# Kernel tuning notes

Hardware: AMD Instinct MI355X
Metric: run time of the kernel (lower is better)

The kernel has to match this reference:

```python
import jax, jax.numpy as jnp
import numpy as np
from jax import lax

KERNEL_SIZE = 15

def _gabor_kernels(theta, sigma, lambd, gamma, psi):
    # Vectorized kernel generation over orientations. Grid is a fixed buffer.
    half = KERNEL_SIZE // 2
    r = jnp.arange(-half, half + 1, dtype=jnp.float32)
    yg, xg = jnp.meshgrid(r, r, indexing='ij')          # [k, k]
    th = theta[:, None, None]                            # [O,1,1]
    sg = jnp.clip(sigma, 1.0, None)[:, None, None]
    lb = jnp.clip(lambd, 2.0, None)[:, None, None]
    gm = jnp.clip(gamma, 0.1, 1.0)[:, None, None]
    ps = psi[:, None, None]
    ct, st = jnp.cos(th), jnp.sin(th)
    x_th = xg * ct + yg * st                             # [O,k,k]
    y_th = -xg * st + yg * ct
    gaussian = jnp.exp(-0.5 * (x_th**2 + gm**2 * y_th**2) / sg**2)
    sinusoid = jnp.cos(2.0 * np.pi * x_th / lb + ps)
    k = gaussian * sinusoid
    k = k - k.mean(axis=(1, 2), keepdims=True)
    # torch.std is unbiased (ddof=1)
    k = k / (k.std(axis=(1, 2), keepdims=True, ddof=1) + 1e-8)
    return k[:, None, :, :]                              # [O,1,k,k]

def setup_inputs() -> dict:
    key = jax.random.key(0)
    O, ks = 8, KERNEL_SIZE
    x = jax.random.normal(key, (64, 3, 256, 256), dtype=jnp.float32)
    theta = jnp.linspace(0.0, np.pi, O + 1)[:-1].astype(jnp.float32)
    sigma = jnp.ones((O,), jnp.float32) * (ks / 4.0)
    lambd = jnp.ones((O,), jnp.float32) * (ks / 2.0)
    gamma = jnp.ones((O,), jnp.float32) * 0.5
    psi = jnp.zeros((O,), jnp.float32)
    return {"x": x, "theta": theta, "sigma": sigma, "lambd": lambd,
            "gamma": gamma, "psi": psi}

def reference(x, theta, sigma, lambd, gamma, psi):
    # sum_i conv2d(x[:,i:i+1], K) == conv2d(sum_i x[:,i:i+1], K) since the
    # same kernels are applied to every channel and conv is linear.
    kernels = _gabor_kernels(theta, sigma, lambd, gamma, psi)  # [O,1,k,k]
    xs = x.sum(axis=1, keepdims=True)                          # [B,1,H,W]
    pad = KERNEL_SIZE // 2
    out = lax.conv_general_dilated(
        xs, kernels,
        window_strides=(1, 1),
        padding=[(pad, pad), (pad, pad)],
        dimension_numbers=('NCHW', 'OIHW', 'NCHW'))
    return out  # [B, O, H, W]
```

## Files before the change

kernel.cpp:

```cpp
#include <hip/hip_runtime.h>
#include <math.h>

#define KS    15
#define HALF  7
#define NORI  8
#define HW    256
#define TW    64
#define TH    64
#define WT    96
#define WROW  48
#define RT    80
#define TWORDS (RT * WROW)

typedef __attribute__((ext_vector_type(8))) short  short8;
typedef __attribute__((ext_vector_type(4))) float  floatx4;

union FragU { uint4 u4; short8 s8; };

__device__ __forceinline__ ushort f2bf(float f) {
    union { float f; uint u; } a; a.f = f;
    return (ushort)((a.u + 0x7FFFu + ((a.u >> 16) & 1u)) >> 16);
}

__global__ __launch_bounds__(256) void gabor_mfma(
    const float* __restrict__ x,
    const float* __restrict__ theta, const float* __restrict__ sigma,
    const float* __restrict__ lambd, const float* __restrict__ gamma,
    const float* __restrict__ psi,
    float* __restrict__ out)
{
    __shared__ uint   tile[2 * TWORDS];
    __shared__ ushort kwa[16 * 16 * 16];

    const int tid  = threadIdx.x;
    const int img  = blockIdx.z;
    const int h0   = blockIdx.y * TH;
    const int w0   = blockIdx.x * TW;
    const int lane = tid & 63;
    const int wave = tid >> 6;

    for (int i = tid; i < 16 * 16 * 16; i += 256) kwa[i] = 0;
    __syncthreads();

    #pragma unroll 1
    for (int oo = 0; oo < 2; ++oo) {
        const int o = wave * 2 + oo;
        const float th = theta[o];
        const float sg = fmaxf(sigma[o], 1.0f);
        const float lb = fmaxf(lambd[o], 2.0f);
        const float gm = fminf(fmaxf(gamma[o], 0.1f), 1.0f);
        const float ps = psi[o];
        const float ct = cosf(th), st = sinf(th);
        const float inv_sg2 = 1.0f / (sg * sg);
        const float gm2 = gm * gm;
        const float wfreq = 6.283185307179586f / lb;

        float vals[4];
        float sum = 0.0f, sumsq = 0.0f;
        #pragma unroll
        for (int j = 0; j < 4; ++j) {
            const int t = lane + j * 64;
            float v = 0.0f;
            if (t < KS * KS) {
                const int ky = t / KS, kx = t % KS;
                const float yg = (float)(ky - HALF);
                const float xg = (float)(kx - HALF);
                const float x_th =  xg * ct + yg * st;
                const float y_th = -xg * st + yg * ct;
                const float g = expf(-0.5f * (x_th * x_th + gm2 * y_th * y_th) * inv_sg2);
                v = g * cosf(wfreq * x_th + ps);
                sum += v; sumsq += v * v;
            }
            vals[j] = v;
        }
        #pragma unroll
        for (int off = 32; off > 0; off >>= 1) {
            sum   += __shfl_down(sum,   off);
            sumsq += __shfl_down(sumsq, off);
        }
        sum = __shfl(sum, 0); sumsq = __shfl(sumsq, 0);
        const float nn   = (float)(KS * KS);
        const float mean = sum / nn;
        const float var  = (sumsq - sum * sum / nn) / (nn - 1.0f);
        const float inv  = 1.0f / (sqrtf(var) + 1e-8f);
        #pragma unroll
        for (int j = 0; j < 4; ++j) {
            const int t = lane + j * 64;
            if (t < KS * KS) {
                const int ky = t / KS, kx = t % KS;
                kwa[(o * 16 + ky) * 16 + kx] = f2bf((vals[j] - mean) * inv);
            }
        }
    }

    {
        const float* xim = x + ((size_t)img * 3) * HW * HW;
        for (int i = tid; i < 2 * TWORDS; i += 256) {
            const int s  = (i >= TWORDS) ? 1 : 0;
            const int j  = i - s * TWORDS;
            const int r  = j / WROW, wc = j - r * WROW;
            const int h  = h0 + r - HALF;
            const int wb = w0 + 2 * wc + s - HALF;
            float v0 = 0.0f, v1 = 0.0f;
            if (h >= 0 && h < HW) {
                const float* xr = xim + h * HW;
                if (wb >= 0 && wb < HW)
                    v0 = xr[wb] + xr[wb + HW * HW] + xr[wb + 2 * HW * HW];
                const int wb1 = wb + 1;
                if (wb1 >= 0 && wb1 < HW)
                    v1 = xr[wb1] + xr[wb1 + HW * HW] + xr[wb1 + 2 * HW * HW];
            }
            tile[i] = (uint)f2bf(v0) | ((uint)f2bf(v1) << 16);
        }
    }
    __syncthreads();

    const int q  = lane >> 4;
    const int n  = lane & 15;
    const int qh = q >> 1;
    const int kx0 = 8 * (q & 1);

    short8 afrag[8];
    #pragma unroll
    for (int c = 0; c < 8; ++c) {
        const int ky = 2 * c + qh;
        afrag[c] = *reinterpret_cast<const short8*>(&kwa[((n * 16 + ky) * 16) + kx0]);
    }

    const int pc   = wave * 16;
    const int col0 = pc + n + kx0;
    const int s    = col0 & 1;
    const int cw   = col0 >> 1;
    const uint cbase = (uint)(s * TWORDS + cw);

    #pragma unroll 1
    for (int it = 0; it < 8; ++it) {
        const int pr0 = it * 8;
        floatx4 acc_e[4], acc_o[4];
        #pragma unroll
        for (int i = 0; i < 4; ++i) { acc_e[i] = (floatx4){0,0,0,0}; acc_o[i] = (floatx4){0,0,0,0}; }

        const uint base0 = cbase + (uint)((pr0 + qh) * WROW);
        #pragma unroll
        for (int t = 0; t < 11; ++t) {
            const uint oe = base0 + (uint)(2 * t * WROW);
            FragU fe, fo;
            fe.u4.x = tile[oe + 0]; fe.u4.y = tile[oe + 1];
            fe.u4.z = tile[oe + 2]; fe.u4.w = tile[oe + 3];
            fo.u4.x = tile[oe + WROW + 0]; fo.u4.y = tile[oe + WROW + 1];
            fo.u4.z = tile[oe + WROW + 2]; fo.u4.w = tile[oe + WROW + 3];
            #pragma unroll
            for (int i = 0; i < 4; ++i) {
                if (t - i >= 0 && t - i < 8) {
                    acc_e[i] = __builtin_amdgcn_mfma_f32_16x16x32_bf16(afrag[t - i], fe.s8, acc_e[i], 0, 0, 0);
                    acc_o[i] = __builtin_amdgcn_mfma_f32_16x16x32_bf16(afrag[t - i], fo.s8, acc_o[i], 0, 0, 0);
                }
            }
        }

        if (q < 2) {
            const int wcol = w0 + pc + n;
            float* ob = out + (((size_t)img * NORI + q * 4) << 16) + wcol;
            #pragma unroll
            for (int i = 0; i < 4; ++i) {
                const int he = h0 + pr0 + 2 * i;
                #pragma unroll
                for (int reg = 0; reg < 4; ++reg) {
                    ob[((size_t)reg << 16) + (he << 8)]       = acc_e[i][reg];
                    ob[((size_t)reg << 16) + ((he + 1) << 8)] = acc_o[i][reg];
                }
            }
        }
    }
}

extern "C" void kernel_launch(void* const* d_in, const int* in_sizes, int n_in,
                              void* d_out, int out_size, void* d_ws, size_t ws_size,
                              hipStream_t stream) {
    const float* x     = (const float*)d_in[0];
    const float* theta = (const float*)d_in[1];
    const float* sigma = (const float*)d_in[2];
    const float* lambd = (const float*)d_in[3];
    const float* gamma = (const float*)d_in[4];
    const float* psi   = (const float*)d_in[5];
    float* out = (float*)d_out;

    dim3 grid(HW / TW, HW / TH, 64);
    gabor_mfma<<<grid, 256, 0, stream>>>(x, theta, sigma, lambd, gamma, psi, out);
}
```

Measured before the change: 208.2 us.

## Pack two output rows per MFMA M-dim and vectorize bf16 tile staging

```diff
diff --git a/kernel.cpp b/kernel.cpp
--- a/kernel.cpp
+++ b/kernel.cpp
@@ -7,10 +7,10 @@
 #define HW    256
 #define TW    64
 #define TH    64
-#define WT    96
 #define WROW  48
 #define RT    80
 #define TWORDS (RT * WROW)
+#define TB1   (TWORDS + 8)
 
 typedef __attribute__((ext_vector_type(8))) short  short8;
 typedef __attribute__((ext_vector_type(4))) float  floatx4;
@@ -21,16 +21,19 @@
     union { float f; uint u; } a; a.f = f;
     return (ushort)((a.u + 0x7FFFu + ((a.u >> 16) & 1u)) >> 16);
 }
-
-__global__ __launch_bounds__(256) void gabor_mfma(
+__device__ __forceinline__ uint pack2(float lo, float hi) {
+    return (uint)f2bf(lo) | ((uint)f2bf(hi) << 16);
+}
+
+__global__ __launch_bounds__(256, 4) void gabor_mfma(
     const float* __restrict__ x,
     const float* __restrict__ theta, const float* __restrict__ sigma,
     const float* __restrict__ lambd, const float* __restrict__ gamma,
     const float* __restrict__ psi,
     float* __restrict__ out)
 {
-    __shared__ uint   tile[2 * TWORDS];
-    __shared__ ushort kwa[16 * 16 * 16];
+    __shared__ uint   tile[2 * TWORDS + 8];
+    __shared__ ushort kwa[NORI * 16 * 16];
 
     const int tid  = threadIdx.x;
     const int img  = blockIdx.z;
@@ -39,7 +42,7 @@
     const int lane = tid & 63;
     const int wave = tid >> 6;
 
-    for (int i = tid; i < 16 * 16 * 16; i += 256) kwa[i] = 0;
+    for (int i = tid; i < NORI * 16 * 16; i += 256) kwa[i] = 0;
     __syncthreads();
 
     #pragma unroll 1
@@ -94,81 +97,101 @@
     }
 
     {
-        const float* xim = x + ((size_t)img * 3) * HW * HW;
-        for (int i = tid; i < 2 * TWORDS; i += 256) {
-            const int s  = (i >= TWORDS) ? 1 : 0;
-            const int j  = i - s * TWORDS;
-            const int r  = j / WROW, wc = j - r * WROW;
+        const float* xim = x + (size_t)img * 3 * HW * HW;
+        for (int slot = tid; slot < RT * 25; slot += 256) {
+            const int r  = slot / 25;
+            const int j  = slot - r * 25;
             const int h  = h0 + r - HALF;
-            const int wb = w0 + 2 * wc + s - HALF;
-            float v0 = 0.0f, v1 = 0.0f;
-            if (h >= 0 && h < HW) {
-                const float* xr = xim + h * HW;
-                if (wb >= 0 && wb < HW)
-                    v0 = xr[wb] + xr[wb + HW * HW] + xr[wb + 2 * HW * HW];
-                const int wb1 = wb + 1;
-                if (wb1 >= 0 && wb1 < HW)
-                    v1 = xr[wb1] + xr[wb1 + HW * HW] + xr[wb1 + 2 * HW * HW];
-            }
-            tile[i] = (uint)f2bf(v0) | ((uint)f2bf(v1) << 16);
+            const int c0 = w0 - 8 + 4 * j;
+            const bool hok = (h >= 0) && (h < HW);
+            const float* xr = xim + h * HW;
+            float s0, s1, s2, s3;
+            if (hok && c0 >= 0 && c0 <= HW - 4) {
+                const float4 a = *(const float4*)&xr[c0];
+                const float4 b = *(const float4*)&xr[c0 + HW * HW];
+                const float4 c = *(const float4*)&xr[c0 + 2 * HW * HW];
+                s0 = a.x + b.x + c.x; s1 = a.y + b.y + c.y;
+                s2 = a.z + b.z + c.z; s3 = a.w + b.w + c.w;
+            } else {
+                s0 = s1 = s2 = s3 = 0.0f;
+                if (hok) {
+                    #pragma unroll
+                    for (int k = 0; k < 4; ++k) {
+                        const int c = c0 + k;
+                        if (c >= 0 && c < HW) {
+                            const float v = xr[c] + xr[c + HW * HW] + xr[c + 2 * HW * HW];
+                            if (k == 0) s0 = v; else if (k == 1) s1 = v;
+                            else if (k == 2) s2 = v; else s3 = v;
+                        }
+                    }
+                }
+            }
+            float s4 = __shfl(s0, lane + 1);
+            if (lane == 63 && j < 24) {
+                const int c = c0 + 4;
+                s4 = 0.0f;
+                if (hok && c >= 0 && c < HW)
+                    s4 = xr[c] + xr[c + HW * HW] + xr[c + 2 * HW * HW];
+            }
+            const int rb = r * WROW;
+            const int w0c = 2 * j;
+            if (w0c < WROW)     tile[rb + w0c]           = pack2(s1, s2);
+            if (w0c + 1 < WROW) tile[rb + w0c + 1]       = pack2(s3, s4);
+            const int w1c = 2 * j - 1;
+            if (w1c >= 0 && w1c < WROW) tile[TB1 + rb + w1c]     = pack2(s0, s1);
+            if (w1c + 1 < WROW)         tile[TB1 + rb + w1c + 1] = pack2(s2, s3);
         }
     }
     __syncthreads();
 
-    const int q  = lane >> 4;
-    const int n  = lane & 15;
-    const int qh = q >> 1;
+    const int q   = lane >> 4;
+    const int n   = lane & 15;
+    const int qh  = q >> 1;
     const int kx0 = 8 * (q & 1);
+    const int o   = n & 7;
+    const int p   = n >> 3;
 
     short8 afrag[8];
     #pragma unroll
     for (int c = 0; c < 8; ++c) {
-        const int ky = 2 * c + qh;
-        afrag[c] = *reinterpret_cast<const short8*>(&kwa[((n * 16 + ky) * 16) + kx0]);
+        const int kyi = (2 * c + qh - p) & 15;
+        afrag[c] = *reinterpret_cast<const short8*>(&kwa[(o * 16 + kyi) * 16 + kx0]);
     }
 
     const int pc   = wave * 16;
     const int col0 = pc + n + kx0;
-    const int s    = col0 & 1;
-    const int cw   = col0 >> 1;
-    const uint cbase = (uint)(s * TWORDS + cw);
+    const uint cbase = (uint)((col0 & 1) * TB1 + (col0 >> 1));
 
     #pragma unroll 1
-    for (int it = 0; it < 8; ++it) {
-        const int pr0 = it * 8;
-        floatx4 acc_e[4], acc_o[4];
-        #pragma unroll
-        for (int i = 0; i < 4; ++i) { acc_e[i] = (floatx4){0,0,0,0}; acc_o[i] = (floatx4){0,0,0,0}; }
-
-        const uint base0 = cbase + (uint)((pr0 + qh) * WROW);
-        #pragma unroll
-        for (int t = 0; t < 11; ++t) {
-            const uint oe = base0 + (uint)(2 * t * WROW);
-            FragU fe, fo;
-            fe.u4.x = tile[oe + 0]; fe.u4.y = tile[oe + 1];
-            fe.u4.z = tile[oe + 2]; fe.u4.w = tile[oe + 3];
-            fo.u4.x = tile[oe + WROW + 0]; fo.u4.y = tile[oe + WROW + 1];
-            fo.u4.z = tile[oe + WROW + 2]; fo.u4.w = tile[oe + WROW + 3];
+    for (int it = 0; it < 4; ++it) {
+        const int pr0 = it * 16;
+        floatx4 acc[8];
+        #pragma unroll
+        for (int i = 0; i < 8; ++i) acc[i] = (floatx4){0, 0, 0, 0};
+
+        const uint rb = cbase + (uint)((pr0 + qh) * WROW);
+        #pragma unroll
+        for (int t = 0; t < 15; ++t) {
+            const uint oe = rb + (uint)(2 * t * WROW);
+            FragU f;
+            f.u4.x = tile[oe];     f.u4.y = tile[oe + 1];
+            f.u4.z = tile[oe + 2]; f.u4.w = tile[oe + 3];
             #pragma unroll
-            for (int i = 0; i < 4; ++i) {
-                if (t - i >= 0 && t - i < 8) {
-                    acc_e[i] = __builtin_amdgcn_mfma_f32_16x16x32_bf16(afrag[t - i], fe.s8, acc_e[i], 0, 0, 0);
-                    acc_o[i] = __builtin_amdgcn_mfma_f32_16x16x32_bf16(afrag[t - i], fo.s8, acc_o[i], 0, 0, 0);
-                }
-            }
-        }
-
-        if (q < 2) {
-            const int wcol = w0 + pc + n;
-            float* ob = out + (((size_t)img * NORI + q * 4) << 16) + wcol;
+            for (int i = 0; i < 8; ++i) {
+                if (t - i >= 0 && t - i < 8)
+                    acc[i] = __builtin_amdgcn_mfma_f32_16x16x32_bf16(afrag[t - i], f.s8, acc[i], 0, 0, 0);
+            }
+        }
+
+        const int wcol = w0 + pc + n;
+        #pragma unroll
+        for (int i = 0; i < 8; ++i) {
+            const int H = h0 + pr0 + 2 * i;
             #pragma unroll
-            for (int i = 0; i < 4; ++i) {
-                const int he = h0 + pr0 + 2 * i;
-                #pragma unroll
-                for (int reg = 0; reg < 4; ++reg) {
-                    ob[((size_t)reg << 16) + (he << 8)]       = acc_e[i][reg];
-                    ob[((size_t)reg << 16) + ((he + 1) << 8)] = acc_o[i][reg];
-                }
+            for (int reg = 0; reg < 4; ++reg) {
+                const int m  = q * 4 + reg;
+                const int om = m & 7, pm = m >> 3;
+                out[(((size_t)img * NORI + om) << 16) + ((size_t)(H + pm) << 8) + wcol] = acc[i][reg];
             }
         }
     }
```

Result: faster. 188.3 us (-9.5%).
